# Optimization experiments

Hardware: AMD Instinct MI355X
Metric: run time of the kernel (lower is better)

Reference implementation:

```python
import jax, jax.numpy as jnp
import numpy as np
from jax import lax

B, C, H, W = 2, 64, 128, 128
NBR, G, K, P, CK = 4, 8, 3, 11, 3
PAD = 6  # (CK-1)//2 + (P-1)//2


def conv2d(x, w, b, pad):
    y = lax.conv_general_dilated(x, w, (1, 1), [(pad, pad), (pad, pad)],
                                 dimension_numbers=('NCHW', 'OIHW', 'NCHW'))
    return y + b[None, :, None, None]


def l2norm(x):
    n = jnp.sqrt(jnp.sum(x * x, axis=1, keepdims=True))
    return x / jnp.maximum(n, 1e-12)


def correlation(f1, f2):
    # spatial correlation sampler: kernel=3, patch=11, stride=1, padding=1
    # corr[b, ph*11+pw, h, w] = sum_{c,ki,kj} f1[b,c,h+ki-1,w+kj-1]*f2[b,c,h+ki-1+ph-5,w+kj-1+pw-5]
    f1p = jnp.pad(f1, ((0, 0), (0, 0), (1, 1), (1, 1)))
    f2p = jnp.pad(f2, ((0, 0), (0, 0), (PAD, PAD), (PAD, PAD)))
    offs = jnp.array([(ph, pw) for ph in range(P) for pw in range(P)], dtype=jnp.int32)

    def one(off):
        sl = lax.dynamic_slice(f2p, (0, 0, off[0], off[1]), (B, C, H + 2, W + 2))
        q = jnp.einsum('bchw,bchw->bhw', f1p, sl)  # (B,H+2,W+2)
        # 3x3 box sum -> (B,H,W)
        return sum(q[:, ki:ki + H, kj:kj + W] for ki in range(CK) for kj in range(CK))

    corr = lax.map(one, offs)  # (121,B,H,W)
    return jnp.transpose(corr, (1, 0, 2, 3))  # (B,121,H,W)


def setup_inputs() -> dict:
    key = jax.random.key(0)
    ks = jax.random.split(key, 12)
    s = 0.05
    return {
        'nbr_fea': jax.random.normal(ks[0], (B, C, H, W), jnp.float32),
        'ref_fea': jax.random.normal(ks[1], (B, C, H, W), jnp.float32),
        'conv1_w': jax.random.normal(ks[2], (C, 2 * C, 3, 3), jnp.float32) * s,
        'conv1_b': jax.random.normal(ks[3], (C,), jnp.float32) * s,
        'conv2_w': jax.random.normal(ks[4], (C, C, 3, 3), jnp.float32) * s,
        'conv2_b': jax.random.normal(ks[5], (C,), jnp.float32) * s,
        'mask_w': jax.random.normal(ks[6], (G * K * K, C, K, K), jnp.float32) * s,
        'mask_b': jax.random.normal(ks[7], (G * K * K,), jnp.float32) * s,
        'nn_w': jax.random.normal(ks[8], (C, NBR * C, 3, 3), jnp.float32) * s,
        'nn_b': jax.random.normal(ks[9], (C,), jnp.float32) * s,
        'agg_w': jax.random.normal(ks[10], (C, 2 * C, 3, 3), jnp.float32) * s,
        'agg_b': jax.random.normal(ks[11], (C,), jnp.float32) * s,
    }


def reference(nbr_fea, ref_fea, conv1_w, conv1_b, conv2_w, conv2_b,
              mask_w, mask_b, nn_w, nn_b, agg_w, agg_b):
    # mask branch
    wf = conv2d(jnp.concatenate([nbr_fea, ref_fea], axis=1), conv1_w, conv1_b, 1)
    wf = conv2d(wf, conv2_w, conv2_b, 1)
    mask = conv2d(wf, mask_w, mask_b, (K - 1) // 2).reshape(B, G, 1, K * K, H, W)

    # local correlation + topk neighbor selection
    corr = correlation(l2norm(ref_fea), l2norm(nbr_fea))  # (B,121,H,W)
    idx = lax.top_k(jnp.transpose(corr, (0, 2, 3, 1)), NBR)[1]  # (B,H,W,NBR)
    ph, pw = idx // P, idx % P

    # gather 3x3 patches centered at displacement (ph-5, pw-5) from pad-6 nbr features
    nbr_pad = jnp.pad(nbr_fea, ((0, 0), (0, 0), (PAD, PAD), (PAD, PAD)))
    r0 = jnp.arange(H)[None, :, None, None] + ph  # (B,H,W,NBR) top-left row in padded img
    c0 = jnp.arange(W)[None, None, :, None] + pw
    ki = jnp.arange(CK)

    def gather_b(fp, r, c):
        R = r[..., None, None] + ki[:, None]   # (H,W,NBR,3,1)
        Cc = c[..., None, None] + ki[None, :]  # (H,W,NBR,1,3)
        return fp[:, R, Cc]  # (C,H,W,NBR,3,3)

    patches = jax.vmap(gather_b)(nbr_pad, r0, c0)  # (B,C,H,W,NBR,3,3)
    L = jnp.transpose(patches, (0, 2, 3, 4, 1, 5, 6)).reshape(B * H * W, NBR * C, CK, CK)
    L = conv2d(L, nn_w, nn_b, 1)  # (B*H*W, C, 3, 3)
    L = L.reshape(B, H, W, C, CK * CK)
    L = jnp.transpose(L, (0, 3, 4, 1, 2)).reshape(B, G, C // G, CK * CK, H, W)

    agg = jnp.sum(L * mask, axis=3).reshape(B, C, H, W)
    agg = jnp.where(agg >= 0, agg, 0.1 * agg)  # LeakyReLU(0.1)
    out = conv2d(jnp.concatenate([agg, ref_fea], axis=1), agg_w, agg_b, 1)
    return out
```

## Files before the change

kernel.cpp:

```cpp
#include <hip/hip_runtime.h>
#include <hip/hip_bf16.h>
#include <math.h>

#define HH 128
#define WW 128
#define HWSZ 16384

typedef __attribute__((ext_vector_type(8))) short short8;
typedef __attribute__((ext_vector_type(4))) float f32x4;

constexpr int OFF_CATT  = 0;
constexpr int OFF_CAT2T = 8388608;
constexpr int OFF_WF1   = 16777216;
constexpr int OFF_WF2   = 20971520;
constexpr int OFF_MASK  = 25165824;
constexpr int OFF_IDX   = 34603008;
constexpr int OFF_WT1   = 35127296;
constexpr int OFF_WT2   = 35274752;
constexpr int OFF_WTM   = 35348480;
constexpr int OFF_WTA   = 35495936;
constexpr int OFF_ZROW  = 35643392;
constexpr int OFF_WB    = 35644416;
constexpr int OFF_F1T   = 38797312;
constexpr int OFF_F2T   = 47185920;
constexpr int OFF_D     = 55574528;
constexpr int OFF_PV    = 71434240;
constexpr int OFF_PP    = 77201408;

__device__ inline ushort f2bf(float f) {
    __hip_bfloat16 h = __float2bfloat16(f);
    return *reinterpret_cast<ushort*>(&h);
}
__device__ inline float bf2f(ushort u) {
    return __uint_as_float(((unsigned)u) << 16);
}

__device__ inline void gload16(const void* g, void* l) {
    __builtin_amdgcn_global_load_lds(
        (const __attribute__((address_space(1))) unsigned int*)g,
        (__attribute__((address_space(3))) unsigned int*)l, 16, 0, 0);
}

__device__ void l2t2_body(int bid, const float* __restrict__ in,
                          float4* __restrict__ normT4,
                          ushort* __restrict__ d1, ushort* __restrict__ d2)
{
    const int pix0 = bid * 64;
    const int b = pix0 >> 14;
    const int hw0 = pix0 & (HWSZ - 1);
    __shared__ float s[64][65];
    __shared__ float sinv[64];
    const int tid = threadIdx.x;
    {
        const int p = tid & 63, c4 = tid >> 6;
#pragma unroll
        for (int r = 0; r < 16; ++r) {
            int c = r * 4 + c4;
            s[c][p] = in[(((size_t)b * 64 + c) << 14) + hw0 + p];
        }
    }
    __syncthreads();
    if (tid < 64) {
        float sum = 0.f;
#pragma unroll
        for (int c = 0; c < 64; ++c) { float v = s[c][tid]; sum = fmaf(v, v, sum); }
        sinv[tid] = 1.f / fmaxf(sqrtf(sum), 1e-12f);
    }
    __syncthreads();
    {
        const int pp = tid & 63, cg = tid >> 6;
        const float inv = sinv[pp];
#pragma unroll
        for (int r = 0; r < 4; ++r) {
            int c4 = cg * 4 + r;
            float4 v = make_float4(s[c4 * 4 + 0][pp] * inv, s[c4 * 4 + 1][pp] * inv,
                                   s[c4 * 4 + 2][pp] * inv, s[c4 * 4 + 3][pp] * inv);
            normT4[(((size_t)b * 16 + c4) << 14) + hw0 + pp] = v;
        }
    }
    {
        const int c = tid & 63, p4 = tid >> 6;
#pragma unroll
        for (int r = 0; r < 16; ++r) {
            int pp = r * 4 + p4;
            ushort bv = f2bf(s[c][pp]);
            d1[(size_t)(pix0 + pp) * 128 + c] = bv;
            if (d2) d2[(size_t)(pix0 + pp) * 128 + c] = bv;
        }
    }
}

__device__ inline ushort wt_elem(const float* __restrict__ w, int Cin, int Cout, int idx) {
    int kc = 9 * Cin;
    int o = idx / kc, rem = idx % kc;
    int tap = rem / Cin, c = rem % Cin;
    float val = (o < Cout) ? w[((size_t)o * Cin + c) * 9 + tap] : 0.f;
    return f2bf(val);
}

__device__ void prep_body(int bid,
                          const float* __restrict__ c1w, const float* __restrict__ c2w,
                          const float* __restrict__ mw,  const float* __restrict__ aw,
                          const float* __restrict__ nnw, char* __restrict__ W)
{
    int gid = bid * 256 + threadIdx.x;
    if (gid < 73728) {
        ((ushort*)(W + OFF_WT1))[gid] = wt_elem(c1w, 128, 64, gid);
    } else if (gid < 110592) {
        int i = gid - 73728;
        ((ushort*)(W + OFF_WT2))[i] = wt_elem(c2w, 64, 64, i);
    } else if (gid < 165888) {
        int i = gid - 110592;
        ((ushort*)(W + OFF_WTM))[i] = wt_elem(mw, 64, 72, i);
    } else if (gid < 239616) {
        int i = gid - 165888;
        ((ushort*)(W + OFF_WTA))[i] = wt_elem(aw, 128, 64, i);
    } else if (gid < 387072) {
        int idx = gid - 239616;
        int j = idx / 36864, rem = idx % 36864;
        int rb = rem >> 6, c = rem & 63;
        int e = rb >> 6, o = rb & 63;
        int ky = e / 3, kx = e % 3;
        ((ushort*)(W + OFF_WB))[idx] =
            f2bf(nnw[(((size_t)o * 256 + j * 64 + c) * 3 + ky) * 3 + kx]);
    } else if (gid < 387200) {
        ((ushort*)(W + OFF_ZROW))[gid - 387072] = 0;
    }
}

__device__ void dot_body(int bid, const float4* __restrict__ f1t4,
                         const float4* __restrict__ f2t4, float* __restrict__ D,
                         const char* __restrict__ zrow, char* __restrict__ sF)
{
    const int q  = bid / 128;
    const int rr = bid % 128;
    const int b  = rr >> 6;
    const int hp = rr & 63;
    const int tid = threadIdx.x;
    const int w = tid & 127, rloc = tid >> 7;
    const int wv = tid >> 6;
    const int h = hp * 2 + rloc;
    const int hw = (h << 7) + w;
    const int y = h + q - 5;
    const bool yok = (unsigned)y < (unsigned)HH;

    float acc[11] = {};
    const float4* f1p = f1t4 + (((size_t)b * 16) << 14) + hw;
    const float4* f2row = f2t4 + (((size_t)b * 16) << 14) + (y << 7) + w;

#pragma unroll 1
    for (int ch = 0; ch < 2; ++ch) {
        const int cb = ch * 8;
#pragma unroll
        for (int i = 0; i < 8; ++i) {
            const void* src = yok ? (const void*)(f2row + ((size_t)(cb + i) << 14))
                                  : (const void*)zrow;
            gload16(src, sF + i * 4096 + wv * 1024);
        }
        __syncthreads();
#pragma unroll
        for (int i = 0; i < 8; ++i) {
            float4 a = f1p[(size_t)(cb + i) << 14];
            const char* base = sF + i * 4096 + rloc * 2048;
#pragma unroll
            for (int pw = 0; pw < 11; ++pw) {
                int x = w + pw - 5;
                if ((unsigned)x < (unsigned)WW) {
                    float4 c = *(const float4*)(base + x * 16);
                    acc[pw] = fmaf(a.x, c.x, acc[pw]);
                    acc[pw] = fmaf(a.y, c.y, acc[pw]);
                    acc[pw] = fmaf(a.z, c.z, acc[pw]);
                    acc[pw] = fmaf(a.w, c.w, acc[pw]);
                }
            }
        }
        __syncthreads();
    }

    float* Dq = D + ((((size_t)b * 121) + q * 11) << 14) + hw;
#pragma unroll
    for (int pw = 0; pw < 11; ++pw) Dq[(size_t)pw << 14] = acc[pw];
}

__device__ void topk_s1_body(int bid, const float* __restrict__ D,
                             float4* __restrict__ Pv, int4* __restrict__ Pp)
{
    const int pix = (bid & 127) * 256 + threadIdx.x;
    const int q = bid >> 7;
    const int b = pix >> 14, hw = pix & (HWSZ - 1), h = hw >> 7, w = hw & 127;
    const int lane = threadIdx.x & 63;
    const float* Db = D + (((size_t)b * 121) << 14);

    float bv[4] = {-1e30f, -1e30f, -1e30f, -1e30f};
    int   bi[4] = {1 << 20, 1 << 20, 1 << 20, 1 << 20};

    for (int pw = 0; pw < 11; ++pw) {
        const int p = q * 11 + pw;
        const float* Dp = Db + ((size_t)p << 14);
        float v = 0.f, vx = 0.f;
#pragma unroll
        for (int dy = -1; dy <= 1; ++dy) {
            int y = h + dy;
            if ((unsigned)y < HH) {
                v += Dp[(y << 7) + w];
                if (lane == 0) { if (w > 0) vx += Dp[(y << 7) + w - 1]; }
                else if (lane == 63) { if (w < 127) vx += Dp[(y << 7) + w + 1]; }
            }
        }
        float vl = __shfl_up(v, 1);
        float vr = __shfl_down(v, 1);
        if (lane == 0)  vl = (w > 0)   ? vx : 0.f;
        if (lane == 63) vr = (w < 127) ? vx : 0.f;
        float s = vl + v + vr;
        if (s > bv[3]) {
            if (s > bv[0]) { bv[3]=bv[2];bi[3]=bi[2]; bv[2]=bv[1];bi[2]=bi[1]; bv[1]=bv[0];bi[1]=bi[0]; bv[0]=s; bi[0]=p; }
            else if (s > bv[1]) { bv[3]=bv[2];bi[3]=bi[2]; bv[2]=bv[1];bi[2]=bi[1]; bv[1]=s; bi[1]=p; }
            else if (s > bv[2]) { bv[3]=bv[2];bi[3]=bi[2]; bv[2]=s; bi[2]=p; }
            else { bv[3]=s; bi[3]=p; }
        }
    }
    Pv[(size_t)q * 32768 + pix] = make_float4(bv[0], bv[1], bv[2], bv[3]);
    Pp[(size_t)q * 32768 + pix] = make_int4(bi[0], bi[1], bi[2], bi[3]);
}

__device__ void topk_s2_body(int bid, const float4* __restrict__ Pv,
                             const int4* __restrict__ Pp, int* __restrict__ idxout)
{
    const int pix = bid * 256 + threadIdx.x;
    float bv2[4] = {-1e30f, -1e30f, -1e30f, -1e30f};
    int   bi2[4] = {1 << 20, 1 << 20, 1 << 20, 1 << 20};
    for (int qq = 0; qq < 11; ++qq) {
        float4 v4 = Pv[(size_t)qq * 32768 + pix];
        int4   p4 = Pp[(size_t)qq * 32768 + pix];
        float vv[4] = {v4.x, v4.y, v4.z, v4.w};
        int   pp4[4] = {p4.x, p4.y, p4.z, p4.w};
#pragma unroll
        for (int r = 0; r < 4; ++r) {
            float v = vv[r]; int pp = pp4[r];
            bool g3 = (v > bv2[3]) || (v == bv2[3] && pp < bi2[3]);
            if (g3) {
                bool g0 = (v > bv2[0]) || (v == bv2[0] && pp < bi2[0]);
                bool g1 = (v > bv2[1]) || (v == bv2[1] && pp < bi2[1]);
                bool g2 = (v > bv2[2]) || (v == bv2[2] && pp < bi2[2]);
                if (g0) { bv2[3]=bv2[2];bi2[3]=bi2[2]; bv2[2]=bv2[1];bi2[2]=bi2[1]; bv2[1]=bv2[0];bi2[1]=bi2[0]; bv2[0]=v; bi2[0]=pp; }
                else if (g1) { bv2[3]=bv2[2];bi2[3]=bi2[2]; bv2[2]=bv2[1];bi2[2]=bi2[1]; bv2[1]=v; bi2[1]=pp; }
                else if (g2) { bv2[3]=bv2[2];bi2[3]=bi2[2]; bv2[2]=v; bi2[2]=pp; }
                else { bv2[3]=v; bi2[3]=pp; }
            }
        }
    }
    int p0 = (bi2[0] / 11) | ((bi2[0] % 11) << 16);
    int p1 = (bi2[1] / 11) | ((bi2[1] % 11) << 16);
    int p2 = (bi2[2] / 11) | ((bi2[2] % 11) << 16);
    int p3 = (bi2[3] / 11) | ((bi2[3] % 11) << 16);
    ((int4*)idxout)[pix] = make_int4(p0, p1, p2, p3);
}

template<int CINPT, int OUTFMT, int BM, int BN, int WN>
__device__ void mmconv_body(int by,
    const char* __restrict__ Wb, int src_off, int rowbytes, int zoff,
    const ushort* __restrict__ WT, int Ktot,
    const float* __restrict__ bias,
    void* __restrict__ outp, int ostride, int nvalid,
    char* __restrict__ sAbuf, char* __restrict__ sBbuf)
{
    constexpr int WM = 4 / WN;
    constexpr int FM = BM / (WM * 16);
    constexpr int FN = BN / (WN * 16);
    constexpr int NA = BM / 32;
    constexpr int NB = BN / 32;
    constexpr int ASZ = BM * 128;
    constexpr int BSZ = BN * 128;
    const int n0 = 0;
    const int m0 = by * BM;
    const int tid = threadIdx.x;
    const int lane = tid & 63, wv = tid >> 6;
    const int lr = lane >> 4, lc = lane & 15;
    const int wr = wv / WN, wc = wv % WN;

    int hA[NA], wA[NA], aBase[NA], swzA[NA];
#pragma unroll
    for (int i = 0; i < NA; ++i) {
        int r  = (i * 4 + wv) * 8 + (lane >> 3);
        int pm = m0 + r;
        int hw = pm & (HWSZ - 1);
        hA[i] = hw >> 7; wA[i] = hw & 127;
        aBase[i] = src_off + (pm >> 14) * (HWSZ * rowbytes);
        swzA[i]  = ((lane & 7) ^ (r & 7)) << 4;
    }
    int boff[NB];
#pragma unroll
    for (int i = 0; i < NB; ++i) {
        int rb = (i * 4 + wv) * 8 + (lane >> 3);
        boff[i] = (n0 + rb) * Ktot * 2 + (((lane & 7) ^ (rb & 7)) << 4);
    }

    f32x4 acc[FM][FN] = {};
    const int NST = Ktot / 64;

#define CSTAGE(S, B)                                                             \
    {                                                                            \
        int k0 = (S) * 64;                                                       \
        int tap = k0 / CINPT;                                                    \
        int c0b = (k0 % CINPT) * 2;                                              \
        int du = tap / 3 - 1, dv = tap % 3 - 1;                                  \
        _Pragma("unroll")                                                        \
        for (int i = 0; i < NA; ++i) {                                           \
            int y = hA[i] + du, x = wA[i] + dv;                                  \
            bool ok = ((unsigned)y < (unsigned)HH) && ((unsigned)x < (unsigned)WW); \
            int off = ok ? (aBase[i] + ((y << 7) + x) * rowbytes + c0b + swzA[i]) : zoff; \
            gload16(Wb + (unsigned)off, sAbuf + (B) * ASZ + (i * 4 + wv) * 1024); \
        }                                                                        \
        _Pragma("unroll")                                                        \
        for (int i = 0; i < NB; ++i)                                             \
            gload16((const char*)WT + (unsigned)(boff[i] + (S) * 128),           \
                    sBbuf + (B) * BSZ + (i * 4 + wv) * 1024);                    \
    }

    CSTAGE(0, 0)
    __syncthreads();
#pragma unroll 1
    for (int s = 0; s < NST; ++s) {
        if (s + 1 < NST) { CSTAGE(s + 1, (s + 1) & 1) }
        const char* cA = sAbuf + (s & 1) * ASZ;
        const char* cB = sBbuf + (s & 1) * BSZ;
#pragma unroll
        for (int ks = 0; ks < 2; ++ks) {
            short8 af[FM]; short8 bfr[FN];
            const int u = ks * 4 + lr;
#pragma unroll
            for (int f = 0; f < FM; ++f) {
                int rr = wr * (FM * 16) + f * 16 + lc;
                af[f] = *(const short8*)&cA[rr * 128 + ((u ^ (rr & 7)) << 4)];
            }
#pragma unroll
            for (int g = 0; g < FN; ++g) {
                int nn = wc * (FN * 16) + g * 16 + lc;
                bfr[g] = *(const short8*)&cB[nn * 128 + ((u ^ (nn & 7)) << 4)];
            }
#pragma unroll
            for (int f = 0; f < FM; ++f)
#pragma unroll
                for (int g = 0; g < FN; ++g)
                    acc[f][g] = __builtin_amdgcn_mfma_f32_16x16x32_bf16(af[f], bfr[g], acc[f][g], 0, 0, 0);
        }
        __syncthreads();
    }
#undef CSTAGE

#pragma unroll
    for (int f = 0; f < FM; ++f)
#pragma unroll
        for (int g = 0; g < FN; ++g) {
            const int col = n0 + wc * (FN * 16) + g * 16 + lc;
            float bv = (bias != nullptr && col < nvalid) ? bias[col] : 0.f;
            if (OUTFMT == 2) {
                const int mb = m0 + wr * (FM * 16) + f * 16 + lr * 4;
                const int bb = mb >> 14, hww = mb & (HWSZ - 1);
                float4 o4 = {acc[f][g][0] + bv, acc[f][g][1] + bv,
                             acc[f][g][2] + bv, acc[f][g][3] + bv};
                *(float4*)((float*)outp + (((size_t)(bb * 64 + col)) << 14) + hww) = o4;
            } else {
#pragma unroll
                for (int reg = 0; reg < 4; ++reg) {
                    const int m = m0 + wr * (FM * 16) + f * 16 + lr * 4 + reg;
                    float v = acc[f][g][reg] + bv;
                    if (OUTFMT == 0)
                        ((ushort*)outp)[(size_t)m * ostride + col] = f2bf(v);
                    else if (col < nvalid)
                        ((float*)outp)[(size_t)m * ostride + col] = v;
                }
            }
        }
}

__global__ __launch_bounds__(256) void k0_prep_l2t2(
    const float* __restrict__ ref, const float* __restrict__ nbr,
    const float* __restrict__ c1w, const float* __restrict__ c2w,
    const float* __restrict__ mw,  const float* __restrict__ aw,
    const float* __restrict__ nnw, char* __restrict__ W)
{
    const int bid = blockIdx.x;
    if (bid < 512) {
        l2t2_body(bid, ref, (float4*)(W + OFF_F1T),
                  (ushort*)(W + OFF_CATT) + 64, (ushort*)(W + OFF_CAT2T) + 64);
    } else if (bid < 1024) {
        l2t2_body(bid - 512, nbr, (float4*)(W + OFF_F2T),
                  (ushort*)(W + OFF_CATT), (ushort*)nullptr);
    } else {
        prep_body(bid - 1024, c1w, c2w, mw, aw, nnw, W);
    }
}

__global__ __launch_bounds__(256) void k1_conv1_dot(
    char* __restrict__ W, const float* __restrict__ c1b)
{
    __shared__ __align__(16) char pool[32768];
    const int bid = blockIdx.x;
    if (bid < 1408) {
        dot_body(bid, (const float4*)(W + OFF_F1T),
                 (const float4*)(W + OFF_F2T), (float*)(W + OFF_D),
                 W + OFF_ZROW, pool);
    } else {
        mmconv_body<128, 0, 32, 64, 4>(bid - 1408, W, OFF_CATT, 256, OFF_ZROW,
            (ushort*)(W + OFF_WT1), 1152, c1b, W + OFF_WF1, 64, 64,
            pool, pool + 8192);
    }
}

__global__ __launch_bounds__(256) void k2_conv2_s1(
    char* __restrict__ W, const float* __restrict__ c2b)
{
    __shared__ __align__(16) char pool[24576];
    const int bid = blockIdx.x;
    if (bid < 1408) {
        topk_s1_body(bid, (const float*)(W + OFF_D),
                     (float4*)(W + OFF_PV), (int4*)(W + OFF_PP));
    } else {
        mmconv_body<64, 0, 32, 64, 4>(bid - 1408, W, OFF_WF1, 128, OFF_ZROW,
            (ushort*)(W + OFF_WT2), 576, c2b, W + OFF_WF2, 64, 64,
            pool, pool + 8192);
    }
}

__global__ __launch_bounds__(256) void k3_convM_s2(
    char* __restrict__ W, const float* __restrict__ mb)
{
    __shared__ __align__(16) char pool[32768];
    const int bid = blockIdx.x;
    if (bid < 1024) {
        mmconv_body<64, 1, 32, 96, 2>(bid, W, OFF_WF2, 128, OFF_ZROW,
            (ushort*)(W + OFF_WTM), 576, mb, (float*)(W + OFF_MASK), 72, 72,
            pool, pool + 8192);
    } else {
        topk_s2_body(bid - 1024, (const float4*)(W + OFF_PV),
                     (const int4*)(W + OFF_PP), (int*)(W + OFF_IDX));
    }
}

__global__ __launch_bounds__(256) void convA_kernel(
    char* __restrict__ W, const float* __restrict__ ab, float* __restrict__ out)
{
    __shared__ __align__(16) char pool[24576];
    mmconv_body<128, 2, 32, 64, 4>(blockIdx.x, W, OFF_CAT2T, 256, OFF_ZROW,
        (ushort*)(W + OFF_WTA), 1152, ab, out, 0, 64, pool, pool + 8192);
}

__global__ __launch_bounds__(256, 3) void patch_kernel(
    const char* __restrict__ Wb, int cat_off, int idx_off, int zoff, int wb_off,
    const float* __restrict__ maskcl, const float* __restrict__ nnb,
    ushort* __restrict__ aggout)
{
    const int m0 = blockIdx.x * 32;
    const int tid = threadIdx.x;
    const int lane = tid & 63, wv = tid >> 6;
    const int lr = lane >> 4, lc = lane & 15;
    const int wr = wv >> 1, wc = wv & 1;

    __shared__ __align__(16) char sP[36864 + 2 * 8192];

    const int r    = tid >> 3;
    const int pm_s = m0 + r;
    const int hw_s = pm_s & (HWSZ - 1);
    const int hS = hw_s >> 7, wS = hw_s & 127;
    const int aBase = cat_off + (pm_s >> 14) * (HWSZ * 256);
    const int swzA  = ((tid & 7) ^ (r & 7)) << 4;
    int bsrc[2];
#pragma unroll
    for (int i = 0; i < 2; ++i) {
        int rl = i * 32 + r;
        bsrc[i] = wb_off + rl * 128 + (((tid & 7) ^ (rl & 7)) << 4);
    }
    const int4 pk4 = ((const int4*)(Wb + idx_off))[pm_s];

    f32x4 acc[9][2] = {};

#define ISSUE_A(PK)                                                              \
    {                                                                            \
        const int hp = hS + ((PK) & 0xffff) - 6;                                 \
        const int wp = wS + ((PK) >> 16) - 6;                                    \
        _Pragma("unroll")                                                        \
        for (int uv = 0; uv < 9; ++uv) {                                         \
            int y = hp + uv / 3, x = wp + uv % 3;                                \
            bool ok = ((unsigned)y < (unsigned)HH) && ((unsigned)x < (unsigned)WW); \
            int off = ok ? (aBase + ((y << 7) + x) * 256 + swzA) : zoff;         \
            gload16(Wb + (unsigned)off, &sP[uv * 4096 + wv * 1024]);             \
        }                                                                        \
    }
#define ISSUE_B1(GE)                                                             \
    {                                                                            \
        const int jj = (GE) / 9, ne = (GE) % 9;                                  \
        _Pragma("unroll")                                                        \
        for (int i = 0; i < 2; ++i)                                              \
            gload16(Wb + (unsigned)(bsrc[i] + jj * 73728 + ne * 8192),           \
                    &sP[36864 + ((GE) & 1) * 8192 + i * 4096 + wv * 1024]);      \
    }

    ISSUE_A(pk4.x)
    ISSUE_B1(0)
    __syncthreads();

#pragma unroll 1
    for (int j = 0; j < 4; ++j) {
        short8 af[9][2];
#pragma unroll
        for (int uv = 0; uv < 9; ++uv)
#pragma unroll
            for (int ks = 0; ks < 2; ++ks) {
                const int rr = wr * 16 + lc;
                af[uv][ks] = *(const short8*)&sP[uv * 4096 + rr * 128 +
                                                (((ks * 4 + lr) ^ (rr & 7)) << 4)];
            }

#pragma unroll
        for (int e = 0; e < 9; ++e) {
            const int ge = j * 9 + e;
            if (e == 1 && j < 3) {
                const int pkn = (j == 0) ? pk4.y : (j == 1) ? pk4.z : pk4.w;
                ISSUE_A(pkn)
            }
            if (ge + 1 < 36) { ISSUE_B1(ge + 1) }

            const char* bt = &sP[36864 + (ge & 1) * 8192];
            short8 bfr[2][2];
#pragma unroll
            for (int gg = 0; gg < 2; ++gg) {
                const int rloc = wc * 32 + gg * 16 + lc;
#pragma unroll
                for (int ks = 0; ks < 2; ++ks)
                    bfr[gg][ks] = *(const short8*)&bt[rloc * 128 +
                                                      (((ks * 4 + lr) ^ (rloc & 7)) << 4)];
            }
            const int ky = e / 3, kx = e % 3;
#pragma unroll
            for (int uv = 0; uv < 9; ++uv) {
                const int uu = uv / 3, vv = uv % 3;
                const int ty = uu - ky + 1, tx = vv - kx + 1;
                if (ty < 0 || ty > 2 || tx < 0 || tx > 2) continue;
                const int t = ty * 3 + tx;
#pragma unroll
                for (int gg = 0; gg < 2; ++gg) {
                    acc[t][gg] = __builtin_amdgcn_mfma_f32_16x16x32_bf16(af[uv][0], bfr[gg][0], acc[t][gg], 0, 0, 0);
                    acc[t][gg] = __builtin_amdgcn_mfma_f32_16x16x32_bf16(af[uv][1], bfr[gg][1], acc[t][gg], 0, 0, 0);
                }
            }
            __syncthreads();
        }
    }
#undef ISSUE_A
#undef ISSUE_B1

#pragma unroll
    for (int gg = 0; gg < 2; ++gg) {
        const int col_o = wc * 32 + gg * 16 + lc;
        const float bo = nnb[col_o];
        const int og = col_o >> 3;
#pragma unroll
        for (int reg = 0; reg < 4; ++reg) {
            const int m = m0 + wr * 16 + lr * 4 + reg;
            const float* mp = maskcl + (size_t)m * 72 + og * 9;
            float s = 0.f;
#pragma unroll
            for (int t = 0; t < 9; ++t) s += (acc[t][gg][reg] + bo) * mp[t];
            s = (s >= 0.f) ? s : 0.1f * s;
            aggout[(size_t)m * 128 + col_o] = f2bf(s);
        }
    }
}

extern "C" void kernel_launch(void* const* d_in, const int* in_sizes, int n_in,
                              void* d_out, int out_size, void* d_ws, size_t ws_size,
                              hipStream_t stream)
{
    const float* nbr = (const float*)d_in[0];
    const float* ref = (const float*)d_in[1];
    const float* c1w = (const float*)d_in[2];
    const float* c1b = (const float*)d_in[3];
    const float* c2w = (const float*)d_in[4];
    const float* c2b = (const float*)d_in[5];
    const float* mw  = (const float*)d_in[6];
    const float* mb  = (const float*)d_in[7];
    const float* nnw = (const float*)d_in[8];
    const float* nnb = (const float*)d_in[9];
    const float* aw  = (const float*)d_in[10];
    const float* ab  = (const float*)d_in[11];
    float* out = (float*)d_out;

    char* W = (char*)d_ws;
    dim3 blk(256);

    k0_prep_l2t2<<<2537, blk, 0, stream>>>(ref, nbr, c1w, c2w, mw, aw, nnw, W);

    k1_conv1_dot<<<2432, blk, 0, stream>>>(W, c1b);

    k2_conv2_s1<<<2432, blk, 0, stream>>>(W, c2b);

    k3_convM_s2<<<1152, blk, 0, stream>>>(W, mb);

    patch_kernel<<<1024, blk, 0, stream>>>(W, OFF_CATT, OFF_IDX, OFF_ZROW, OFF_WB,
                                           (const float*)(W + OFF_MASK), nnb,
                                           (ushort*)(W + OFF_CAT2T));

    convA_kernel<<<1024, blk, 0, stream>>>(W, ab, out);
}
```

Measured before the change: 153.7 us.

## Load patch-conv weights directly from global memory and cut LDS footprint

```diff
diff --git a/kernel.cpp b/kernel.cpp
--- a/kernel.cpp
+++ b/kernel.cpp
@@ -446,7 +446,7 @@
         (ushort*)(W + OFF_WTA), 1152, ab, out, 0, 64, pool, pool + 8192);
 }
 
-__global__ __launch_bounds__(256, 3) void patch_kernel(
+__global__ __launch_bounds__(256, 4) void patch_kernel(
     const char* __restrict__ Wb, int cat_off, int idx_off, int zoff, int wb_off,
     const float* __restrict__ maskcl, const float* __restrict__ nnb,
     ushort* __restrict__ aggout)
@@ -457,7 +457,7 @@
     const int lr = lane >> 4, lc = lane & 15;
     const int wr = wv >> 1, wc = wv & 1;
 
-    __shared__ __align__(16) char sP[36864 + 2 * 8192];
+    __shared__ __align__(16) char sA[36864];
 
     const int r    = tid >> 3;
     const int pm_s = m0 + r;
@@ -465,13 +465,9 @@
     const int hS = hw_s >> 7, wS = hw_s & 127;
     const int aBase = cat_off + (pm_s >> 14) * (HWSZ * 256);
     const int swzA  = ((tid & 7) ^ (r & 7)) << 4;
-    int bsrc[2];
-#pragma unroll
-    for (int i = 0; i < 2; ++i) {
-        int rl = i * 32 + r;
-        bsrc[i] = wb_off + rl * 128 + (((tid & 7) ^ (rl & 7)) << 4);
-    }
     const int4 pk4 = ((const int4*)(Wb + idx_off))[pm_s];
+
+    const char* wbt = Wb + wb_off + (wc * 32 + lc) * 128 + lr * 16;
 
     f32x4 acc[9][2] = {};
 
@@ -484,53 +480,34 @@
             int y = hp + uv / 3, x = wp + uv % 3;                                \
             bool ok = ((unsigned)y < (unsigned)HH) && ((unsigned)x < (unsigned)WW); \
             int off = ok ? (aBase + ((y << 7) + x) * 256 + swzA) : zoff;         \
-            gload16(Wb + (unsigned)off, &sP[uv * 4096 + wv * 1024]);             \
+            gload16(Wb + (unsigned)off, &sA[uv * 4096 + wv * 1024]);             \
         }                                                                        \
     }
-#define ISSUE_B1(GE)                                                             \
-    {                                                                            \
-        const int jj = (GE) / 9, ne = (GE) % 9;                                  \
-        _Pragma("unroll")                                                        \
-        for (int i = 0; i < 2; ++i)                                              \
-            gload16(Wb + (unsigned)(bsrc[i] + jj * 73728 + ne * 8192),           \
-                    &sP[36864 + ((GE) & 1) * 8192 + i * 4096 + wv * 1024]);      \
-    }
 
     ISSUE_A(pk4.x)
-    ISSUE_B1(0)
     __syncthreads();
 
 #pragma unroll 1
     for (int j = 0; j < 4; ++j) {
-        short8 af[9][2];
-#pragma unroll
-        for (int uv = 0; uv < 9; ++uv)
-#pragma unroll
-            for (int ks = 0; ks < 2; ++ks) {
-                const int rr = wr * 16 + lc;
-                af[uv][ks] = *(const short8*)&sP[uv * 4096 + rr * 128 +
-                                                (((ks * 4 + lr) ^ (rr & 7)) << 4)];
-            }
-
+        const char* wbj = wbt + j * 73728;
 #pragma unroll
         for (int e = 0; e < 9; ++e) {
-            const int ge = j * 9 + e;
-            if (e == 1 && j < 3) {
-                const int pkn = (j == 0) ? pk4.y : (j == 1) ? pk4.z : pk4.w;
-                ISSUE_A(pkn)
-            }
-            if (ge + 1 < 36) { ISSUE_B1(ge + 1) }
-
-            const char* bt = &sP[36864 + (ge & 1) * 8192];
+            short8 af[9][2];
+#pragma unroll
+            for (int uv = 0; uv < 9; ++uv)
+#pragma unroll
+                for (int ks = 0; ks < 2; ++ks) {
+                    const int rr = wr * 16 + lc;
+                    af[uv][ks] = *(const short8*)&sA[uv * 4096 + rr * 128 +
+                                                    (((ks * 4 + lr) ^ (rr & 7)) << 4)];
+                }
             short8 bfr[2][2];
 #pragma unroll
-            for (int gg = 0; gg < 2; ++gg) {
-                const int rloc = wc * 32 + gg * 16 + lc;
+            for (int gg = 0; gg < 2; ++gg)
 #pragma unroll
                 for (int ks = 0; ks < 2; ++ks)
-                    bfr[gg][ks] = *(const short8*)&bt[rloc * 128 +
-                                                      (((ks * 4 + lr) ^ (rloc & 7)) << 4)];
-            }
+                    bfr[gg][ks] = *(const short8*)(wbj + e * 8192 + gg * 2048 + ks * 64);
+
             const int ky = e / 3, kx = e % 3;
 #pragma unroll
             for (int uv = 0; uv < 9; ++uv) {
@@ -544,11 +521,15 @@
                     acc[t][gg] = __builtin_amdgcn_mfma_f32_16x16x32_bf16(af[uv][1], bfr[gg][1], acc[t][gg], 0, 0, 0);
                 }
             }
+        }
+        if (j < 3) {
             __syncthreads();
+            const int pkn = (j == 0) ? pk4.y : (j == 1) ? pk4.z : pk4.w;
+            ISSUE_A(pkn)
+            __syncthreads();
         }
     }
 #undef ISSUE_A
-#undef ISSUE_B1
 
 #pragma unroll
     for (int gg = 0; gg < 2; ++gg) {
```

New measurement: 277.5 us. 1.81x slower.
